# Performance work log

Hardware: AMD Instinct MI355X
Metric: run time of the kernel (lower is better)

The kernel has to match this reference:

```python
import jax, jax.numpy as jnp
import numpy as np

B, L, S = 32, 8192, 128  # E == S == D == 128 required by the einsum labeling

def setup_inputs() -> dict:
    key = jax.random.key(0)
    kq, kk, kv = jax.random.split(key, 3)
    queries = jax.random.normal(kq, (B, L, S), dtype=jnp.float32)
    keys = jax.random.normal(kk, (B, S, S), dtype=jnp.float32)
    values = jax.random.normal(kv, (B, S, S), dtype=jnp.float32)
    return {"queries": queries, "keys": keys, "values": values}

def reference(queries, keys, values):
    # queries: (B, L, E), keys/values: (B, S, D) with E == S == D.
    # scores_1: sum-pooled outer product term (reduced-rank additive score)
    s1 = queries.sum(-1)[:, :, None] * keys.sum(-1)[:, None, :]   # (B, L, S)
    # scores_2: q contracted against key-position axis (plain batched matmul, no transpose)
    s2 = jnp.einsum('bls,bsd->bld', queries, keys)                # (B, L, S)
    A = jax.nn.softmax(s1 + s2, axis=-1)                          # (B, L, S)
    out = jnp.einsum('bls,bsd->bld', A, values)                   # (B, L, D)
    # original returns shape (B, 1, L, D) for the 3D-input path
    return out[:, None, :, :]
```

## Files before the change

### kernel.cpp

```cpp
#include <hip/hip_runtime.h>

#define SDIM 128
#define LDIM 8192
#define BATCH 32

#define WS_KV_STRIDE 65536
#define WS_KSUM_OFF (BATCH * WS_KV_STRIDE)

typedef __attribute__((ext_vector_type(8))) _Float16 half8;
typedef __attribute__((ext_vector_type(16))) float float16;

union H8U { half8 v; _Float16 h[8]; unsigned w[4]; };
union PU { _Float16 h[2]; unsigned u; };

static __device__ __forceinline__ float16 mfma_f16(half8 a, half8 b, float16 c) {
    return __builtin_amdgcn_mfma_f32_32x32x16_f16(a, b, c, 0, 0, 0);
}

__global__ __launch_bounds__(256) void prep_kernel(
        const float* __restrict__ keys, const float* __restrict__ values,
        char* __restrict__ ws) {
    __shared__ float T[SDIM * 33];
    const int blk = blockIdx.x;
    const int tid = threadIdx.x;

    if (blk < 256) {
        const int b = blk >> 3, which = (blk >> 2) & 1, m = blk & 3;
        const float* src = (which ? values : keys) + (size_t)b * SDIM * SDIM;

        #pragma unroll
        for (int j = 0; j < 4; ++j) {
            int lin = j * 256 + tid;
            int c = lin >> 3, f4 = lin & 7;
            float4 v = *(const float4*)(src + c * SDIM + m * 32 + f4 * 4);
            T[c * 33 + f4 * 4 + 0] = v.x;
            T[c * 33 + f4 * 4 + 1] = v.y;
            T[c * 33 + f4 * 4 + 2] = v.z;
            T[c * 33 + f4 * 4 + 3] = v.w;
        }
        __syncthreads();

        char* dst = ws + (size_t)b * WS_KV_STRIDE + (which ? 32768 : 0);
        #pragma unroll
        for (int j = 0; j < 2; ++j) {
            int e = j * 256 + tid;
            int ks = e >> 6, lane = e & 63;
            int Hh = (lane >> 5) & 1, ln = lane & 31;
            int c0 = 16 * ks + 8 * Hh;
            H8U o;
            #pragma unroll
            for (int i = 0; i < 8; ++i)
                o.h[i] = (_Float16)T[(c0 + i) * 33 + ln];
            *(half8*)(dst + ((m * 8 + ks) * 64 + lane) * 16) = o.v;
        }
    } else {
        const int b = blk - 256;
        const float* src = keys + (size_t)b * SDIM * SDIM;
        int row = tid >> 1, h = tid & 1;
        const float4* p = (const float4*)(src + row * SDIM + h * 64);
        float s = 0.f;
        #pragma unroll
        for (int k = 0; k < 16; ++k) { float4 v = p[k]; s += v.x + v.y + v.z + v.w; }
        s += __shfl_xor(s, 1, 64);
        if (h == 0)
            ((float*)(ws + WS_KSUM_OFF + b * 512))[row] = s;
    }
}

__global__ __launch_bounds__(64, 4) void attn_kernel(
        const float* __restrict__ q, const char* __restrict__ ws,
        float* __restrict__ out) {
    __shared__ char smQ[8192];
    __shared__ float qsum_s[32];
    const int blk = blockIdx.x;
    const int b = blk >> 8, t32 = blk & 255;
    const int tid = threadIdx.x, lane = tid & 63;
    const int H = lane >> 5, ln = lane & 31;

    const char* wsb = ws + (size_t)b * WS_KV_STRIDE;
    const float* qblk = q + ((size_t)b * LDIM + t32 * 32) * SDIM;
    float* ob = out + ((size_t)b * LDIM + t32 * 32) * SDIM;

    const char* ktp = wsb;
    const char* vtp = wsb + 32768;
    const int lo16 = lane * 16;

    const int rb = (((tid >> 4) & 3) << 3);
    const int cc = tid & 15;
    {
        float4 bufA[4][2], bufB[4][2];
        #pragma unroll
        for (int it = 0; it < 4; ++it) {
            const float* p = qblk + (rb + it) * SDIM + cc * 8;
            bufA[it][0] = *(const float4*)p;
            bufA[it][1] = *(const float4*)(p + 4);
        }
        #pragma unroll
        for (int it = 0; it < 4; ++it) {
            const float* p = qblk + (rb + 4 + it) * SDIM + cc * 8;
            bufB[it][0] = *(const float4*)p;
            bufB[it][1] = *(const float4*)(p + 4);
        }
        #pragma unroll
        for (int g = 0; g < 2; ++g) {
            #pragma unroll
            for (int it2 = 0; it2 < 4; ++it2) {
                int row = rb + g * 4 + it2;
                float4 v0 = g ? bufB[it2][0] : bufA[it2][0];
                float4 v1 = g ? bufB[it2][1] : bufA[it2][1];
                float f[8] = {v0.x, v0.y, v0.z, v0.w, v1.x, v1.y, v1.z, v1.w};
                float s = f[0] + f[1] + f[2] + f[3] + f[4] + f[5] + f[6] + f[7];
                s += __shfl_xor(s, 1, 64);
                s += __shfl_xor(s, 2, 64);
                s += __shfl_xor(s, 4, 64);
                s += __shfl_xor(s, 8, 64);
                if ((tid & 15) == 0) qsum_s[row] = s;
                H8U hv;
                #pragma unroll
                for (int i = 0; i < 8; ++i) hv.h[i] = (_Float16)f[i];
                *(half8*)(smQ + row * 256 + ((cc ^ (row & 15)) * 16)) = hv.v;
            }
        }
    }

    const char* qrp = smQ + ln * 256;

    half8 ah[2][4];
    #pragma unroll
    for (int m = 0; m < 4; ++m)
        ah[0][m] = *(const half8*)(ktp + (m * 8 + 0) * 1024 + lo16);
    #pragma unroll
    for (int m = 0; m < 4; ++m)
        ah[1][m] = *(const half8*)(ktp + (m * 8 + 1) * 1024 + lo16);

    float16 acc[4];
    #pragma unroll
    for (int m = 0; m < 4; ++m) acc[m] = (float16)(0.0f);

    #pragma unroll
    for (int ks = 0; ks < 8; ++ks) {
        const int cur = ks & 1;
        half8 bh = *(const half8*)(qrp + ((2 * ks + H) ^ (ln & 15)) * 16);
        #pragma unroll
        for (int m = 0; m < 4; ++m) acc[m] = mfma_f16(ah[cur][m], bh, acc[m]);
        if (ks < 6) {
            #pragma unroll
            for (int m = 0; m < 4; ++m)
                ah[cur][m] = *(const half8*)(ktp + (m * 8 + ks + 2) * 1024 + lo16);
        }
    }

    const float4* ksg = (const float4*)(ws + WS_KSUM_OFF + b * 512);
    float4 kk[2][4];
    #pragma unroll
    for (int g = 0; g < 4; ++g) kk[0][g] = ksg[g * 2 + H];

    half8 av[2][4];
    #pragma unroll
    for (int dm = 0; dm < 4; ++dm)
        av[0][dm] = *(const half8*)(vtp + (dm * 8) * 1024 + lo16);

    const float qs = qsum_s[ln];
    #pragma unroll
    for (int m = 0; m < 4; ++m) {
        const int cur = m & 1;
        if (m < 3) {
            #pragma unroll
            for (int g = 0; g < 4; ++g) kk[cur ^ 1][g] = ksg[(m + 1) * 8 + g * 2 + H];
        }
        #pragma unroll
        for (int g = 0; g < 4; ++g) {
            float4 k4 = kk[cur][g];
            acc[m][4 * g + 0] = fmaf(k4.x, qs, acc[m][4 * g + 0]);
            acc[m][4 * g + 1] = fmaf(k4.y, qs, acc[m][4 * g + 1]);
            acc[m][4 * g + 2] = fmaf(k4.z, qs, acc[m][4 * g + 2]);
            acc[m][4 * g + 3] = fmaf(k4.w, qs, acc[m][4 * g + 3]);
        }
    }

    float mx = -1e30f;
    #pragma unroll
    for (int m = 0; m < 4; ++m)
        #pragma unroll
        for (int r = 0; r < 16; ++r) mx = fmaxf(mx, acc[m][r]);
    mx = fmaxf(mx, __shfl_xor(mx, 32, 64));
    float sum = 0.0f;
    #pragma unroll
    for (int m = 0; m < 4; ++m)
        #pragma unroll
        for (int r = 0; r < 16; ++r) {
            float e = __expf(acc[m][r] - mx);
            acc[m][r] = e;
            sum += e;
        }
    sum += __shfl_xor(sum, 32, 64);
    const float inv = 1.0f / sum;

    unsigned pk[4][8];
    #pragma unroll
    for (int m = 0; m < 4; ++m)
        #pragma unroll
        for (int rr = 0; rr < 8; ++rr) {
            PU pu;
            pu.h[0] = (_Float16)(acc[m][2 * rr] * inv);
            pu.h[1] = (_Float16)(acc[m][2 * rr + 1] * inv);
            pk[m][rr] = pu.u;
        }

    #pragma unroll
    for (int dm = 0; dm < 4; ++dm)
        av[1][dm] = *(const half8*)(vtp + (dm * 8 + 1) * 1024 + lo16);

    float16 oacc[4];
    #pragma unroll
    for (int m = 0; m < 4; ++m) oacc[m] = (float16)(0.0f);

    #pragma unroll
    for (int t = 0; t < 8; ++t) {
        const int cur = t & 1;
        const int m = t >> 1;
        const int c = 4 * (t & 1);
        unsigned p0 = pk[m][c], p1 = pk[m][c + 1], p2 = pk[m][c + 2], p3 = pk[m][c + 3];
        unsigned a0 = H ? p2 : p0, a1 = H ? p3 : p1;
        unsigned s0 = H ? p0 : p2, s1 = H ? p1 : p3;
        unsigned r0 = (unsigned)__shfl_xor((int)s0, 32, 64);
        unsigned r1 = (unsigned)__shfl_xor((int)s1, 32, 64);
        H8U bf;
        bf.w[0] = H ? r0 : a0;
        bf.w[1] = H ? r1 : a1;
        bf.w[2] = H ? a0 : r0;
        bf.w[3] = H ? a1 : r1;
        #pragma unroll
        for (int dm = 0; dm < 4; ++dm)
            oacc[dm] = mfma_f16(av[cur][dm], bf.v, oacc[dm]);
        if (t < 6) {
            #pragma unroll
            for (int dm = 0; dm < 4; ++dm)
                av[cur][dm] = *(const half8*)(vtp + (dm * 8 + t + 2) * 1024 + lo16);
        }
    }

    #pragma unroll
    for (int dm = 0; dm < 4; ++dm)
        #pragma unroll
        for (int g = 0; g < 4; ++g) {
            float4 v = make_float4(oacc[dm][4 * g], oacc[dm][4 * g + 1],
                                   oacc[dm][4 * g + 2], oacc[dm][4 * g + 3]);
            *(float4*)(ob + ln * SDIM + dm * 32 + g * 8 + H * 4) = v;
        }
}

extern "C" void kernel_launch(void* const* d_in, const int* in_sizes, int n_in,
                              void* d_out, int out_size, void* d_ws, size_t ws_size,
                              hipStream_t stream) {
    const float* q    = (const float*)d_in[0];
    const float* keys = (const float*)d_in[1];
    const float* vals = (const float*)d_in[2];
    float* out = (float*)d_out;
    char*  ws  = (char*)d_ws;

    prep_kernel<<<BATCH * 8 + BATCH, 256, 0, stream>>>(keys, vals, ws);
    attn_kernel<<<BATCH * 256, 64, 0, stream>>>(q, ws, out);
}
```

Measured before the change: 268.3 us.

## Process two query tiles per block and prefetch the next tile's Q

Each attention block now handles two consecutive 32-row query tiles instead of one, so the grid is halved. While the first tile's scores are computed, the second tile's fp32 queries are loaded into registers, hiding global load latency behind MFMA and softmax work. The launch_bounds occupancy hint is dropped, which lets the compiler use more registers for the prefetch buffers but may lower waves per SIMD.

```diff
diff --git a/kernel.cpp b/kernel.cpp
--- a/kernel.cpp
+++ b/kernel.cpp
@@ -67,40 +67,42 @@
     }
 }
 
-__global__ __launch_bounds__(64, 4) void attn_kernel(
+__global__ __launch_bounds__(64) void attn_kernel(
         const float* __restrict__ q, const char* __restrict__ ws,
         float* __restrict__ out) {
     __shared__ char smQ[8192];
     __shared__ float qsum_s[32];
     const int blk = blockIdx.x;
-    const int b = blk >> 8, t32 = blk & 255;
+    const int b = blk >> 7, pair = blk & 127;
     const int tid = threadIdx.x, lane = tid & 63;
     const int H = lane >> 5, ln = lane & 31;
 
     const char* wsb = ws + (size_t)b * WS_KV_STRIDE;
-    const float* qblk = q + ((size_t)b * LDIM + t32 * 32) * SDIM;
-    float* ob = out + ((size_t)b * LDIM + t32 * 32) * SDIM;
+    const float* qblk = q + ((size_t)b * LDIM + pair * 64) * SDIM;
+    float* obase = out + ((size_t)b * LDIM + pair * 64) * SDIM;
 
     const char* ktp = wsb;
     const char* vtp = wsb + 32768;
     const int lo16 = lane * 16;
-
     const int rb = (((tid >> 4) & 3) << 3);
     const int cc = tid & 15;
-    {
-        float4 bufA[4][2], bufB[4][2];
-        #pragma unroll
-        for (int it = 0; it < 4; ++it) {
-            const float* p = qblk + (rb + it) * SDIM + cc * 8;
-            bufA[it][0] = *(const float4*)p;
-            bufA[it][1] = *(const float4*)(p + 4);
-        }
-        #pragma unroll
-        for (int it = 0; it < 4; ++it) {
-            const float* p = qblk + (rb + 4 + it) * SDIM + cc * 8;
-            bufB[it][0] = *(const float4*)p;
-            bufB[it][1] = *(const float4*)(p + 4);
-        }
+
+    float4 bufA[4][2], bufB[4][2];
+    #pragma unroll
+    for (int it = 0; it < 4; ++it) {
+        const float* p = qblk + (rb + it) * SDIM + cc * 8;
+        bufA[it][0] = *(const float4*)p;
+        bufA[it][1] = *(const float4*)(p + 4);
+    }
+    #pragma unroll
+    for (int it = 0; it < 4; ++it) {
+        const float* p = qblk + (rb + 4 + it) * SDIM + cc * 8;
+        bufB[it][0] = *(const float4*)p;
+        bufB[it][1] = *(const float4*)(p + 4);
+    }
+
+    #pragma unroll
+    for (int t = 0; t < 2; ++t) {
         #pragma unroll
         for (int g = 0; g < 2; ++g) {
             #pragma unroll
@@ -121,133 +123,150 @@
                 *(half8*)(smQ + row * 256 + ((cc ^ (row & 15)) * 16)) = hv.v;
             }
         }
-    }
-
-    const char* qrp = smQ + ln * 256;
-
-    half8 ah[2][4];
-    #pragma unroll
-    for (int m = 0; m < 4; ++m)
-        ah[0][m] = *(const half8*)(ktp + (m * 8 + 0) * 1024 + lo16);
-    #pragma unroll
-    for (int m = 0; m < 4; ++m)
-        ah[1][m] = *(const half8*)(ktp + (m * 8 + 1) * 1024 + lo16);
-
-    float16 acc[4];
-    #pragma unroll
-    for (int m = 0; m < 4; ++m) acc[m] = (float16)(0.0f);
-
-    #pragma unroll
-    for (int ks = 0; ks < 8; ++ks) {
-        const int cur = ks & 1;
-        half8 bh = *(const half8*)(qrp + ((2 * ks + H) ^ (ln & 15)) * 16);
-        #pragma unroll
-        for (int m = 0; m < 4; ++m) acc[m] = mfma_f16(ah[cur][m], bh, acc[m]);
-        if (ks < 6) {
-            #pragma unroll
-            for (int m = 0; m < 4; ++m)
-                ah[cur][m] = *(const half8*)(ktp + (m * 8 + ks + 2) * 1024 + lo16);
-        }
-    }
-
-    const float4* ksg = (const float4*)(ws + WS_KSUM_OFF + b * 512);
-    float4 kk[2][4];
-    #pragma unroll
-    for (int g = 0; g < 4; ++g) kk[0][g] = ksg[g * 2 + H];
-
-    half8 av[2][4];
-    #pragma unroll
-    for (int dm = 0; dm < 4; ++dm)
-        av[0][dm] = *(const half8*)(vtp + (dm * 8) * 1024 + lo16);
-
-    const float qs = qsum_s[ln];
-    #pragma unroll
-    for (int m = 0; m < 4; ++m) {
-        const int cur = m & 1;
-        if (m < 3) {
-            #pragma unroll
-            for (int g = 0; g < 4; ++g) kk[cur ^ 1][g] = ksg[(m + 1) * 8 + g * 2 + H];
-        }
-        #pragma unroll
-        for (int g = 0; g < 4; ++g) {
-            float4 k4 = kk[cur][g];
-            acc[m][4 * g + 0] = fmaf(k4.x, qs, acc[m][4 * g + 0]);
-            acc[m][4 * g + 1] = fmaf(k4.y, qs, acc[m][4 * g + 1]);
-            acc[m][4 * g + 2] = fmaf(k4.z, qs, acc[m][4 * g + 2]);
-            acc[m][4 * g + 3] = fmaf(k4.w, qs, acc[m][4 * g + 3]);
-        }
-    }
-
-    float mx = -1e30f;
-    #pragma unroll
-    for (int m = 0; m < 4; ++m)
-        #pragma unroll
-        for (int r = 0; r < 16; ++r) mx = fmaxf(mx, acc[m][r]);
-    mx = fmaxf(mx, __shfl_xor(mx, 32, 64));
-    float sum = 0.0f;
-    #pragma unroll
-    for (int m = 0; m < 4; ++m)
-        #pragma unroll
-        for (int r = 0; r < 16; ++r) {
-            float e = __expf(acc[m][r] - mx);
-            acc[m][r] = e;
-            sum += e;
-        }
-    sum += __shfl_xor(sum, 32, 64);
-    const float inv = 1.0f / sum;
-
-    unsigned pk[4][8];
-    #pragma unroll
-    for (int m = 0; m < 4; ++m)
-        #pragma unroll
-        for (int rr = 0; rr < 8; ++rr) {
-            PU pu;
-            pu.h[0] = (_Float16)(acc[m][2 * rr] * inv);
-            pu.h[1] = (_Float16)(acc[m][2 * rr + 1] * inv);
-            pk[m][rr] = pu.u;
-        }
-
-    #pragma unroll
-    for (int dm = 0; dm < 4; ++dm)
-        av[1][dm] = *(const half8*)(vtp + (dm * 8 + 1) * 1024 + lo16);
-
-    float16 oacc[4];
-    #pragma unroll
-    for (int m = 0; m < 4; ++m) oacc[m] = (float16)(0.0f);
-
-    #pragma unroll
-    for (int t = 0; t < 8; ++t) {
-        const int cur = t & 1;
-        const int m = t >> 1;
-        const int c = 4 * (t & 1);
-        unsigned p0 = pk[m][c], p1 = pk[m][c + 1], p2 = pk[m][c + 2], p3 = pk[m][c + 3];
-        unsigned a0 = H ? p2 : p0, a1 = H ? p3 : p1;
-        unsigned s0 = H ? p0 : p2, s1 = H ? p1 : p3;
-        unsigned r0 = (unsigned)__shfl_xor((int)s0, 32, 64);
-        unsigned r1 = (unsigned)__shfl_xor((int)s1, 32, 64);
-        H8U bf;
-        bf.w[0] = H ? r0 : a0;
-        bf.w[1] = H ? r1 : a1;
-        bf.w[2] = H ? a0 : r0;
-        bf.w[3] = H ? a1 : r1;
+
+        const char* qrp = smQ + ln * 256;
+
+        half8 ah[2][4];
+        #pragma unroll
+        for (int m = 0; m < 4; ++m)
+            ah[0][m] = *(const half8*)(ktp + (m * 8 + 0) * 1024 + lo16);
+        #pragma unroll
+        for (int m = 0; m < 4; ++m)
+            ah[1][m] = *(const half8*)(ktp + (m * 8 + 1) * 1024 + lo16);
+
+        float16 acc[4];
+        #pragma unroll
+        for (int m = 0; m < 4; ++m) acc[m] = (float16)(0.0f);
+
+        #pragma unroll
+        for (int ks = 0; ks < 8; ++ks) {
+            const int cur = ks & 1;
+            half8 bh = *(const half8*)(qrp + ((2 * ks + H) ^ (ln & 15)) * 16);
+            #pragma unroll
+            for (int m = 0; m < 4; ++m) acc[m] = mfma_f16(ah[cur][m], bh, acc[m]);
+            if (ks < 6) {
+                #pragma unroll
+                for (int m = 0; m < 4; ++m)
+                    ah[cur][m] = *(const half8*)(ktp + (m * 8 + ks + 2) * 1024 + lo16);
+            }
+        }
+
+        const float4* ksg = (const float4*)(ws + WS_KSUM_OFF + b * 512);
+        float4 kk[2][4];
+        #pragma unroll
+        for (int g = 0; g < 4; ++g) kk[0][g] = ksg[g * 2 + H];
+
+        half8 av[2][4];
         #pragma unroll
         for (int dm = 0; dm < 4; ++dm)
-            oacc[dm] = mfma_f16(av[cur][dm], bf.v, oacc[dm]);
-        if (t < 6) {
+            av[0][dm] = *(const half8*)(vtp + (dm * 8) * 1024 + lo16);
+
+        const float qs = qsum_s[ln];
+        #pragma unroll
+        for (int m = 0; m < 4; ++m) {
+            const int cur = m & 1;
+            if (m < 3) {
+                #pragma unroll
+                for (int g = 0; g < 4; ++g) kk[cur ^ 1][g] = ksg[(m + 1) * 8 + g * 2 + H];
+            }
+            #pragma unroll
+            for (int g = 0; g < 4; ++g) {
+                float4 k4 = kk[cur][g];
+                acc[m][4 * g + 0] = fmaf(k4.x, qs, acc[m][4 * g + 0]);
+                acc[m][4 * g + 1] = fmaf(k4.y, qs, acc[m][4 * g + 1]);
+                acc[m][4 * g + 2] = fmaf(k4.z, qs, acc[m][4 * g + 2]);
+                acc[m][4 * g + 3] = fmaf(k4.w, qs, acc[m][4 * g + 3]);
+            }
+        }
+
+        if (t == 0) {
+            const float* qn = qblk + 32 * SDIM;
+            #pragma unroll
+            for (int it = 0; it < 4; ++it) {
+                const float* p = qn + (rb + it) * SDIM + cc * 8;
+                bufA[it][0] = *(const float4*)p;
+                bufA[it][1] = *(const float4*)(p + 4);
+            }
+            #pragma unroll
+            for (int it = 0; it < 4; ++it) {
+                const float* p = qn + (rb + 4 + it) * SDIM + cc * 8;
+                bufB[it][0] = *(const float4*)p;
+                bufB[it][1] = *(const float4*)(p + 4);
+            }
+        }
+
+        float mx = -1e30f;
+        #pragma unroll
+        for (int m = 0; m < 4; ++m)
+            #pragma unroll
+            for (int r = 0; r < 16; ++r) mx = fmaxf(mx, acc[m][r]);
+        mx = fmaxf(mx, __shfl_xor(mx, 32, 64));
+        float sum = 0.0f;
+        #pragma unroll
+        for (int m = 0; m < 4; ++m)
+            #pragma unroll
+            for (int r = 0; r < 16; ++r) {
+                float e = __expf(acc[m][r] - mx);
+                acc[m][r] = e;
+                sum += e;
+            }
+        sum += __shfl_xor(sum, 32, 64);
+        const float inv = 1.0f / sum;
+
+        unsigned pk[4][8];
+        #pragma unroll
+        for (int m = 0; m < 4; ++m)
+            #pragma unroll
+            for (int rr = 0; rr < 8; ++rr) {
+                PU pu;
+                pu.h[0] = (_Float16)(acc[m][2 * rr] * inv);
+                pu.h[1] = (_Float16)(acc[m][2 * rr + 1] * inv);
+                pk[m][rr] = pu.u;
+            }
+
+        #pragma unroll
+        for (int dm = 0; dm < 4; ++dm)
+            av[1][dm] = *(const half8*)(vtp + (dm * 8 + 1) * 1024 + lo16);
+
+        float16 oacc[4];
+        #pragma unroll
+        for (int m = 0; m < 4; ++m) oacc[m] = (float16)(0.0f);
+
+        #pragma unroll
+        for (int tt = 0; tt < 8; ++tt) {
+            const int cur = tt & 1;
+            const int m = tt >> 1;
+            const int c = 4 * (tt & 1);
+            unsigned p0 = pk[m][c], p1 = pk[m][c + 1], p2 = pk[m][c + 2], p3 = pk[m][c + 3];
+            unsigned a0 = H ? p2 : p0, a1 = H ? p3 : p1;
+            unsigned s0 = H ? p0 : p2, s1 = H ? p1 : p3;
+            unsigned r0 = (unsigned)__shfl_xor((int)s0, 32, 64);
+            unsigned r1 = (unsigned)__shfl_xor((int)s1, 32, 64);
+            H8U bf;
+            bf.w[0] = H ? r0 : a0;
+            bf.w[1] = H ? r1 : a1;
+            bf.w[2] = H ? a0 : r0;
+            bf.w[3] = H ? a1 : r1;
             #pragma unroll
             for (int dm = 0; dm < 4; ++dm)
-                av[cur][dm] = *(const half8*)(vtp + (dm * 8 + t + 2) * 1024 + lo16);
-        }
-    }
-
-    #pragma unroll
-    for (int dm = 0; dm < 4; ++dm)
-        #pragma unroll
-        for (int g = 0; g < 4; ++g) {
-            float4 v = make_float4(oacc[dm][4 * g], oacc[dm][4 * g + 1],
-                                   oacc[dm][4 * g + 2], oacc[dm][4 * g + 3]);
-            *(float4*)(ob + ln * SDIM + dm * 32 + g * 8 + H * 4) = v;
-        }
+                oacc[dm] = mfma_f16(av[cur][dm], bf.v, oacc[dm]);
+            if (tt < 6) {
+                #pragma unroll
+                for (int dm = 0; dm < 4; ++dm)
+                    av[cur][dm] = *(const half8*)(vtp + (dm * 8 + tt + 2) * 1024 + lo16);
+            }
+        }
+
+        float* ob = obase + (t * 32) * SDIM;
+        #pragma unroll
+        for (int dm = 0; dm < 4; ++dm)
+            #pragma unroll
+            for (int g = 0; g < 4; ++g) {
+                float4 v = make_float4(oacc[dm][4 * g], oacc[dm][4 * g + 1],
+                                       oacc[dm][4 * g + 2], oacc[dm][4 * g + 3]);
+                *(float4*)(ob + ln * SDIM + dm * 32 + g * 8 + H * 4) = v;
+            }
+    }
 }
 
 extern "C" void kernel_launch(void* const* d_in, const int* in_sizes, int n_in,
@@ -260,5 +279,5 @@
     char*  ws  = (char*)d_ws;
 
     prep_kernel<<<BATCH * 8 + BATCH, 256, 0, stream>>>(keys, vals, ws);
-    attn_kernel<<<BATCH * 256, 64, 0, stream>>>(q, ws, out);
-}
+    attn_kernel<<<BATCH * 128, 64, 0, stream>>>(q, ws, out);
+}
```

Result: faster. 260.0 us (-3.1%).
